# Optimization experiments

Measured on AMD Instinct MI355X. Metric: run time of the kernel, lower is better.

The kernel has to match this reference:

```python
import jax, jax.numpy as jnp
import numpy as np

B, CIN, COUT, K, H, W = 8, 512, 512, 3, 64, 64
SCALE = 1.0 / np.sqrt(CIN * K * K).astype(np.float32)  # conv.scale
LRELU_SCALE = 1.4142135623730951  # sqrt(2), FusedLeakyReLU scale


def setup_inputs() -> dict:
    key = jax.random.key(0)
    ks = jax.random.split(key, 6)
    return {
        "x": jax.random.normal(ks[0], (B, CIN, H, W), jnp.float32),
        "style": jax.random.normal(ks[1], (B, CIN), jnp.float32),
        "noise": jax.random.normal(ks[2], (1, 1, H, W), jnp.float32),
        "weight": jax.random.normal(ks[3], (COUT, CIN, K, K), jnp.float32),
        "bias": jnp.zeros((COUT,), jnp.float32),
        "noise_strength": jax.random.uniform(ks[4], (1,), jnp.float32),
    }


def reference(x, style, noise, weight, bias, noise_strength):
    # Modulate: scale * weight * style  -> [B, Cout, Cin, K, K]
    w = SCALE * weight[None] * style[:, None, :, None, None]
    # Demodulate per (batch, out_channel)
    demod = jax.lax.rsqrt(jnp.sum(w * w, axis=(2, 3, 4)) + 1e-8)
    w = w * demod[:, :, None, None, None]
    # Per-sample conv (grouped-conv trick in torch) via vmap over batch
    pad = K // 2
    def conv_one(xi, wi):  # xi: [Cin,H,W], wi: [Cout,Cin,K,K]
        return jax.lax.conv_general_dilated(
            xi[None], wi, window_strides=(1, 1),
            padding=[(pad, pad), (pad, pad)],
            dimension_numbers=("NCHW", "OIHW", "NCHW"))[0]
    out = jax.vmap(conv_one)(x, w)  # [B, Cout, H, W]
    # NoiseInjection: out + strength * noise (noise broadcast over B, C)
    out = out + noise_strength[0] * noise
    # FusedLeakyReLU: leaky_relu(out + bias, 0.2) * sqrt(2)
    y = out + bias[None, :, None, None]
    return jnp.where(y >= 0, y, 0.2 * y) * LRELU_SCALE
```

## Files before the change

kernel.cpp:

```cpp
#include <hip/hip_runtime.h>
#include <hip/hip_bf16.h>

typedef __attribute__((ext_vector_type(8))) short s16x8;
typedef __attribute__((ext_vector_type(16))) float f32x16;

#define MOD_SCALE 0.014731391274719739f

__device__ __forceinline__ void gload_lds16(const void* g, void* l) {
    __builtin_amdgcn_global_load_lds(
        (const __attribute__((address_space(1))) unsigned int*)g,
        (__attribute__((address_space(3))) unsigned int*)l, 16, 0, 0);
}

__device__ __forceinline__ void sync_drain() {
    __builtin_amdgcn_s_waitcnt(0);
    __syncthreads();
}

__global__ __launch_bounds__(256) void k_prep(const float* __restrict__ x,
                                              const float* __restrict__ style,
                                              const float* __restrict__ weight,
                                              __hip_bfloat16* __restrict__ xs,
                                              __hip_bfloat16* __restrict__ wb,
                                              float* __restrict__ dem) {
    __shared__ __align__(16) char sm[71680];
    const int t = threadIdx.x;
    const int bid = blockIdx.x;

    if (bid < 520) {
        const int idx = bid * 256 + t;
        const int b = idx / 16640;
        const int r2 = idx - b * 16640;
        const int cb = r2 / 1040;
        const int r3 = r2 - cb * 1040;
        const int pair = r3 >> 2;
        const int chunk = r3 & 3;
        int pr, pc;
        if (pair < 66)       { pr = 0;          pc = pair; }
        else if (pair < 132) { pr = 65;         pc = pair - 66; }
        else if (pair < 196) { pr = pair - 131; pc = 0; }
        else                 { pr = pair - 195; pc = 65; }
        char* d = (char*)xs +
                  ((size_t)(b * 16 + cb) * 4356 + pr * 66 + pc) * 64 +
                  chunk * 16;
        *(uint4*)d = make_uint4(0u, 0u, 0u, 0u);
    } else if (bid < 1032) {
        const int r = bid - 520;
        const int b = r >> 6, h = r & 63;
        __hip_bfloat16 (*tile)[68] = (__hip_bfloat16(*)[68])sm;
        float* sf = (float*)(sm + 69632);
        sf[t] = style[b * 512 + t] * MOD_SCALE;
        sf[t + 256] = style[b * 512 + 256 + t] * MOD_SCALE;
        __syncthreads();
        const float* xb = x + (size_t)b * 512 * 4096 + h * 64;
#pragma unroll 4
        for (int it = 0; it < 32; ++it) {
            int idx = it * 256 + t;
            int ci = idx >> 4, w4 = idx & 15;
            float4 v = *(const float4*)(xb + (size_t)ci * 4096 + w4 * 4);
            float s = sf[ci];
            union { uint2 u2; __hip_bfloat16 q[4]; } pk;
            pk.q[0] = __float2bfloat16(v.x * s);
            pk.q[1] = __float2bfloat16(v.y * s);
            pk.q[2] = __float2bfloat16(v.z * s);
            pk.q[3] = __float2bfloat16(v.w * s);
            *(uint2*)&tile[ci][w4 * 4] = pk.u2;
        }
        __syncthreads();
        const int cig = t & 3, w = t >> 2;
        char* ob = (char*)xs + (size_t)b * 4460544 +
                   (size_t)((h + 1) * 66 + 1) * 64;
#pragma unroll
        for (int cb = 0; cb < 16; ++cb) {
            union { uint4 u; __hip_bfloat16 q[8]; } pk;
#pragma unroll
            for (int j = 0; j < 8; ++j)
                pk.q[j] = tile[cb * 32 + cig * 8 + j][w];
            *(uint4*)(ob + (size_t)cb * 278784 + w * 64 + cig * 16) = pk.u;
        }
    } else if (bid < 2056) {
        const int r = bid - 1032;
        float* lds = (float*)sm;
        const int p0 = r * 256;
        const float* src = weight + (size_t)p0 * 9;
#pragma unroll
        for (int k = 0; k < 9; ++k) lds[k * 256 + t] = src[k * 256 + t];
        __syncthreads();
#pragma unroll
        for (int tap = 0; tap < 9; ++tap)
            wb[(size_t)tap * 262144 + p0 + t] = __float2bfloat16(lds[t * 9 + tap]);
    } else {
        const int co = bid - 2056;
        float* s2 = (float*)sm;
        for (int i = t; i < 4096; i += 256) { float v = style[i]; s2[i] = v * v; }
        __syncthreads();
        const float4* wp = (const float4*)(weight + (size_t)co * 4608);
        float acc[8] = {0.f, 0.f, 0.f, 0.f, 0.f, 0.f, 0.f, 0.f};
        for (int j = t; j < 1152; j += 256) {
            float4 v = wp[j];
            float w2[4] = {v.x * v.x, v.y * v.y, v.z * v.z, v.w * v.w};
            int base = j * 4;
#pragma unroll
            for (int e = 0; e < 4; ++e) {
                int ci = (base + e) / 9;
                float ww = w2[e];
#pragma unroll
                for (int bb = 0; bb < 8; ++bb) acc[bb] += ww * s2[bb * 512 + ci];
            }
        }
#pragma unroll
        for (int bb = 0; bb < 8; ++bb)
            for (int off = 32; off > 0; off >>= 1)
                acc[bb] += __shfl_down(acc[bb], off);
        float* red = (float*)(sm + 16384);
        const int wv = t >> 6, lane = t & 63;
        if (lane == 0) {
#pragma unroll
            for (int bb = 0; bb < 8; ++bb) red[wv * 8 + bb] = acc[bb];
        }
        __syncthreads();
        if (t < 8) {
            float s = red[t] + red[8 + t] + red[16 + t] + red[24 + t];
            const float S2 = MOD_SCALE * MOD_SCALE;
            dem[t * 512 + co] = rsqrtf(S2 * s + 1e-8f);
        }
    }
}

__global__ __launch_bounds__(256, 2) void k_conv(
    const __hip_bfloat16* __restrict__ xs,
    const __hip_bfloat16* __restrict__ wb,
    const float* __restrict__ demod,
    const float* __restrict__ noise,
    const float* __restrict__ bias,
    const float* __restrict__ nstr,
    float* __restrict__ out) {
    __shared__ __align__(16) char Xl[25344];
    __shared__ __align__(16) char Wl[6][8192];

    const int t = threadIdx.x;
    const int bi = blockIdx.x;
    const int spat = bi & 127;
    const int b = spat >> 4;
    const int h0 = (spat & 15) << 2;
    const int co0 = (bi >> 7) << 7;
    const int lane = t & 63;
    const int wv = t >> 6;
    const int wm = wv & 1, wn = wv >> 1;
    const int el = lane & 31;
    const int hk = lane >> 5;

    f32x16 acc[2][4];
#pragma unroll
    for (int i = 0; i < 2; ++i)
#pragma unroll
        for (int j = 0; j < 4; ++j)
#pragma unroll
            for (int k = 0; k < 16; ++k) acc[i][j][k] = 0.f;

    const char* xsb = (const char*)xs + (size_t)b * 4460544;
    const char* xsrc[7];
#pragma unroll
    for (int i = 0; i < 6; ++i) {
        int g = i * 256 + t;
        int e = g >> 2, s = g & 3;
        int gc = (s - (e >> 2)) & 3;
        int row = e / 66, col = e - row * 66;
        xsrc[i] = xsb + (size_t)((h0 + row) * 66 + col) * 64 + gc * 16;
    }
    {
        int g = 1536 + t;
        int e = g >> 2, s = g & 3;
        int gc = (s - (e >> 2)) & 3;
        int row = e / 66, col = e - row * 66;
        xsrc[6] = xsb + (size_t)((h0 + row) * 66 + col) * 64 + gc * 16;
    }
    const char* wsrc[2];
#pragma unroll
    for (int i = 0; i < 2; ++i) {
        int g = i * 256 + t;
        int e = g >> 2, s = g & 3;
        int gc = (s - (e >> 2)) & 3;
        wsrc[i] = (const char*)wb + (size_t)(co0 + e) * 1024 + gc * 16;
    }
    const int wvoff = wv << 10;

#pragma unroll
    for (int i = 0; i < 6; ++i) gload_lds16(xsrc[i], Xl + i * 4096 + wvoff);
    if (t < 48) gload_lds16(xsrc[6], Xl + 24576);
#pragma unroll
    for (int tt = 0; tt < 3; ++tt)
#pragma unroll
        for (int i = 0; i < 2; ++i)
            gload_lds16(wsrc[i] + (size_t)tt * 524288,
                        Wl[tt] + i * 4096 + wvoff);
    sync_drain();

    int cboff = 0;
    for (int cb = 0; cb < 16; ++cb, cboff += 64) {
        const int ncboff = (cb < 15) ? cboff + 64 : cboff;
#pragma unroll
        for (int p = 0; p < 3; ++p) {
            const int bank = ((cb + p) & 1) * 3;
            const int nbank = 3 - bank;
#pragma unroll
            for (int tt = 0; tt < 3; ++tt) {
                const size_t soff = (p < 2)
                    ? (size_t)(3 * (p + 1) + tt) * 524288 + cboff
                    : (size_t)tt * 524288 + ncboff;
                char* dst = Wl[nbank + tt] + wvoff;
#pragma unroll
                for (int i = 0; i < 2; ++i)
                    gload_lds16(wsrc[i] + soff, dst + i * 4096);
            }
#pragma unroll
            for (int tt = 0; tt < 3; ++tt) {
                const char* Wb = Wl[bank + tt];
#pragma unroll
                for (int ks = 0; ks < 2; ++ks) {
                    const int c = 2 * ks + hk;
                    s16x8 af[2], bfr[4];
#pragma unroll
                    for (int mi = 0; mi < 2; ++mi) {
                        int e = wm * 64 + mi * 32 + el;
                        af[mi] = *(const s16x8*)(Wb + e * 64 +
                                                 (((c + (e >> 2)) & 3) << 4));
                    }
#pragma unroll
                    for (int ni = 0; ni < 4; ++ni) {
                        int e = (2 * wn + (ni >> 1) + p) * 66 + tt +
                                (ni & 1) * 32 + el;
                        bfr[ni] = *(const s16x8*)(Xl + e * 64 +
                                                  (((c + (e >> 2)) & 3) << 4));
                    }
#pragma unroll
                    for (int mi = 0; mi < 2; ++mi)
#pragma unroll
                        for (int ni = 0; ni < 4; ++ni)
                            acc[mi][ni] =
                                __builtin_amdgcn_mfma_f32_32x32x16_bf16(
                                    af[mi], bfr[ni], acc[mi][ni], 0, 0, 0);
                }
            }
            sync_drain();
        }
        if (cb < 15) {
            const size_t xo = (size_t)(cb + 1) * 278784;
#pragma unroll
            for (int i = 0; i < 6; ++i)
                gload_lds16(xsrc[i] + xo, Xl + i * 4096 + wvoff);
            if (t < 48) gload_lds16(xsrc[6] + xo, Xl + 24576);
            sync_drain();
        }
    }

    const float nsv = nstr[0];
    const float LR = 1.4142135623730951f;
#pragma unroll
    for (int mi = 0; mi < 2; ++mi) {
        float dm[16], bs[16];
#pragma unroll
        for (int rg = 0; rg < 16; ++rg) {
            int co = co0 + wm * 64 + mi * 32 + (rg & 3) + 8 * (rg >> 2) + 4 * hk;
            dm[rg] = demod[b * 512 + co];
            bs[rg] = bias[co];
        }
#pragma unroll
        for (int ni = 0; ni < 4; ++ni) {
            int h = h0 + 2 * wn + (ni >> 1);
            int w = (ni & 1) * 32 + el;
            float nz = nsv * noise[h * 64 + w];
#pragma unroll
            for (int rg = 0; rg < 16; ++rg) {
                int co = co0 + wm * 64 + mi * 32 + (rg & 3) + 8 * (rg >> 2) +
                         4 * hk;
                float v = acc[mi][ni][rg] * dm[rg] + nz + bs[rg];
                v = (v >= 0.f ? v : 0.2f * v) * LR;
                out[(((size_t)b * 512 + co) * 64 + h) * 64 + w] = v;
            }
        }
    }
}

extern "C" void kernel_launch(void* const* d_in, const int* in_sizes, int n_in,
                              void* d_out, int out_size, void* d_ws, size_t ws_size,
                              hipStream_t stream) {
    const float* x      = (const float*)d_in[0];
    const float* style  = (const float*)d_in[1];
    const float* noise  = (const float*)d_in[2];
    const float* weight = (const float*)d_in[3];
    const float* bias   = (const float*)d_in[4];
    const float* nstr   = (const float*)d_in[5];
    float* out = (float*)d_out;

    char* ws = (char*)d_ws;
    __hip_bfloat16* xs = (__hip_bfloat16*)ws;
    __hip_bfloat16* wb = (__hip_bfloat16*)(ws + 35684352);
    float* demod = (float*)(ws + 35684352 + 4718592);

    k_prep<<<2568, 256, 0, stream>>>(x, style, weight, xs, wb, demod);
    k_conv<<<512, 256, 0, stream>>>(xs, wb, demod, noise, bias, nstr, out);
}
```

Baseline: 252.6 us.

## Split input prep into separate kernel with smaller LDS tiles

The input modulation/transpose work moves out of the combined prep kernel into its own kernel. Each block now handles 64 channels by 4 rows (33 KB LDS) instead of all 512 channels of one row (70 KB LDS). The weight conversion, halo zeroing and demod blocks go into a second kernel whose LDS drops to about 17 KB. The goal is higher occupancy and smaller LDS footprints in the prep phase, at the cost of one extra kernel launch.

```diff
diff --git a/kernel.cpp b/kernel.cpp
--- a/kernel.cpp
+++ b/kernel.cpp
@@ -17,13 +17,65 @@
     __syncthreads();
 }
 
-__global__ __launch_bounds__(256) void k_prep(const float* __restrict__ x,
-                                              const float* __restrict__ style,
-                                              const float* __restrict__ weight,
-                                              __hip_bfloat16* __restrict__ xs,
-                                              __hip_bfloat16* __restrict__ wb,
-                                              float* __restrict__ dem) {
-    __shared__ __align__(16) char sm[71680];
+__global__ __launch_bounds__(256) void k_xprep(const float* __restrict__ x,
+                                               const float* __restrict__ style,
+                                               __hip_bfloat16* __restrict__ xs) {
+    __shared__ __align__(16) char sm[33280];
+    const int t = threadIdx.x;
+    const int bid = blockIdx.x;
+    const int b = bid >> 7;
+    const int r = bid & 127;
+    const int hq = r >> 3, cie = r & 7;
+    const int ci0 = cie * 64, h0 = hq * 4;
+
+    __hip_bfloat16 (*tile)[258] = (__hip_bfloat16(*)[258])sm;
+    float* sf = (float*)(sm + 33024);
+    if (t < 64) sf[t] = style[b * 512 + ci0 + t] * MOD_SCALE;
+    __syncthreads();
+
+    const float* xb = x + ((size_t)(b * 512 + ci0) * 64 + h0) * 64;
+#pragma unroll 4
+    for (int it = 0; it < 16; ++it) {
+        int idx = it * 256 + t;
+        int ci = idx >> 6, c4 = idx & 63;
+        float4 v = *(const float4*)(xb + (size_t)ci * 4096 + c4 * 4);
+        float s = sf[ci];
+        union { unsigned u[2]; __hip_bfloat16 q[4]; } pk;
+        pk.q[0] = __float2bfloat16(v.x * s);
+        pk.q[1] = __float2bfloat16(v.y * s);
+        pk.q[2] = __float2bfloat16(v.z * s);
+        pk.q[3] = __float2bfloat16(v.w * s);
+        char* d = (char*)sm + ci * 516 + c4 * 8;
+        *(unsigned*)d = pk.u[0];
+        *(unsigned*)(d + 4) = pk.u[1];
+    }
+    __syncthreads();
+
+    const int cig = t & 3, w = t >> 2;
+    char* xsb = (char*)xs + (size_t)b * 4460544;
+#pragma unroll
+    for (int cbL = 0; cbL < 2; ++cbL) {
+        const size_t cbo = (size_t)(cie * 2 + cbL) * 278784;
+#pragma unroll
+        for (int hr = 0; hr < 4; ++hr) {
+            const int sp = hr * 64 + w;
+            union { uint4 u; __hip_bfloat16 q[8]; } pk;
+#pragma unroll
+            for (int j = 0; j < 8; ++j)
+                pk.q[j] = tile[cbL * 32 + cig * 8 + j][sp];
+            *(uint4*)(xsb + cbo +
+                      (size_t)((h0 + hr + 1) * 66 + (w + 1)) * 64 +
+                      cig * 16) = pk.u;
+        }
+    }
+}
+
+__global__ __launch_bounds__(256) void k_aux(const float* __restrict__ style,
+                                             const float* __restrict__ weight,
+                                             __hip_bfloat16* __restrict__ xs,
+                                             __hip_bfloat16* __restrict__ wb,
+                                             float* __restrict__ dem) {
+    __shared__ __align__(16) char sm[16896];
     const int t = threadIdx.x;
     const int bid = blockIdx.x;
 
@@ -44,42 +96,8 @@
                   ((size_t)(b * 16 + cb) * 4356 + pr * 66 + pc) * 64 +
                   chunk * 16;
         *(uint4*)d = make_uint4(0u, 0u, 0u, 0u);
-    } else if (bid < 1032) {
+    } else if (bid < 1544) {
         const int r = bid - 520;
-        const int b = r >> 6, h = r & 63;
-        __hip_bfloat16 (*tile)[68] = (__hip_bfloat16(*)[68])sm;
-        float* sf = (float*)(sm + 69632);
-        sf[t] = style[b * 512 + t] * MOD_SCALE;
-        sf[t + 256] = style[b * 512 + 256 + t] * MOD_SCALE;
-        __syncthreads();
-        const float* xb = x + (size_t)b * 512 * 4096 + h * 64;
-#pragma unroll 4
-        for (int it = 0; it < 32; ++it) {
-            int idx = it * 256 + t;
-            int ci = idx >> 4, w4 = idx & 15;
-            float4 v = *(const float4*)(xb + (size_t)ci * 4096 + w4 * 4);
-            float s = sf[ci];
-            union { uint2 u2; __hip_bfloat16 q[4]; } pk;
-            pk.q[0] = __float2bfloat16(v.x * s);
-            pk.q[1] = __float2bfloat16(v.y * s);
-            pk.q[2] = __float2bfloat16(v.z * s);
-            pk.q[3] = __float2bfloat16(v.w * s);
-            *(uint2*)&tile[ci][w4 * 4] = pk.u2;
-        }
-        __syncthreads();
-        const int cig = t & 3, w = t >> 2;
-        char* ob = (char*)xs + (size_t)b * 4460544 +
-                   (size_t)((h + 1) * 66 + 1) * 64;
-#pragma unroll
-        for (int cb = 0; cb < 16; ++cb) {
-            union { uint4 u; __hip_bfloat16 q[8]; } pk;
-#pragma unroll
-            for (int j = 0; j < 8; ++j)
-                pk.q[j] = tile[cb * 32 + cig * 8 + j][w];
-            *(uint4*)(ob + (size_t)cb * 278784 + w * 64 + cig * 16) = pk.u;
-        }
-    } else if (bid < 2056) {
-        const int r = bid - 1032;
         float* lds = (float*)sm;
         const int p0 = r * 256;
         const float* src = weight + (size_t)p0 * 9;
@@ -90,7 +108,7 @@
         for (int tap = 0; tap < 9; ++tap)
             wb[(size_t)tap * 262144 + p0 + t] = __float2bfloat16(lds[t * 9 + tap]);
     } else {
-        const int co = bid - 2056;
+        const int co = bid - 1544;
         float* s2 = (float*)sm;
         for (int i = t; i < 4096; i += 256) { float v = style[i]; s2[i] = v * v; }
         __syncthreads();
@@ -298,6 +316,7 @@
     __hip_bfloat16* wb = (__hip_bfloat16*)(ws + 35684352);
     float* demod = (float*)(ws + 35684352 + 4718592);
 
-    k_prep<<<2568, 256, 0, stream>>>(x, style, weight, xs, wb, demod);
+    k_xprep<<<1024, 256, 0, stream>>>(x, style, xs);
+    k_aux<<<2056, 256, 0, stream>>>(style, weight, xs, wb, demod);
     k_conv<<<512, 256, 0, stream>>>(xs, wb, demod, noise, bias, nstr, out);
 }
```

After: 257.1 us. Within noise of the previous version (+1.8%).
